# Performance work log

Measured on AMD Instinct MI355X. Metric: run time of the kernel, lower is better.

## Reference

```python
import jax, jax.numpy as jnp
import numpy as np

D_MODEL, N_HEADS, D_K, D_V, D_FF, N_LAYERS = 512, 8, 64, 64, 2048, 6
NEG = -1e9
EPS = 1e-5


def layernorm(x):
    # nn.LayerNorm(d_model) created fresh each call: weight=1, bias=0
    mu = jnp.mean(x, axis=-1, keepdims=True)
    var = jnp.var(x, axis=-1, keepdims=True)
    return (x - mu) * jax.lax.rsqrt(var + EPS)


def sinusoidal_pe(seq_len, d_model, dtype=jnp.float32):
    pos = np.arange(seq_len)[:, None].astype(np.float64)
    div = np.exp(np.arange(0, d_model, 2).astype(np.float64) * (-np.log(10000.0) / d_model))
    pe = np.zeros((seq_len, d_model))
    pe[:, 0::2] = np.sin(pos * div)
    pe[:, 1::2] = np.cos(pos * div)
    return jnp.asarray(pe, dtype=dtype)


def mha(q_in, k_in, v_in, mask, Wq, Wk, Wv, Wo):
    # q_in: [B,Lq,D]; k_in/v_in: [B,Lk,D]; mask: [B,Lq,Lk] bool (True = masked)
    B, Lq, _ = q_in.shape
    Lk = k_in.shape[1]
    Q = (q_in @ Wq).reshape(B, Lq, N_HEADS, D_K).transpose(0, 2, 1, 3)
    K = (k_in @ Wk).reshape(B, Lk, N_HEADS, D_K).transpose(0, 2, 1, 3)
    V = (v_in @ Wv).reshape(B, Lk, N_HEADS, D_V).transpose(0, 2, 1, 3)
    scores = jnp.einsum('bhqd,bhkd->bhqk', Q, K) / jnp.sqrt(jnp.asarray(D_K, q_in.dtype))
    scores = jnp.where(mask[:, None, :, :], jnp.asarray(NEG, scores.dtype), scores)
    attn = jax.nn.softmax(scores, axis=-1)
    ctx = jnp.einsum('bhqk,bhkd->bhqd', attn, V)
    ctx = ctx.transpose(0, 2, 1, 3).reshape(B, Lq, N_HEADS * D_V)
    return layernorm(ctx @ Wo + q_in)


def setup_inputs() -> dict:
    key = jax.random.key(0)
    ks = jax.random.split(key, 16)
    B, T, S, V = 8, 1024, 1024, 32000
    s = 0.02
    inp = {
        'dec_inputs': jax.random.randint(ks[0], (B, T), 0, V),
        'enc_inputs': jax.random.randint(ks[1], (B, S), 0, V),
        'enc_outputs': jax.random.normal(ks[2], (B, S, D_MODEL), jnp.float32),
        'emb': jax.random.normal(ks[3], (V, D_MODEL), jnp.float32) * s,
        'Wq_self': jax.random.normal(ks[4], (N_LAYERS, D_MODEL, N_HEADS * D_K), jnp.float32) * s,
        'Wk_self': jax.random.normal(ks[5], (N_LAYERS, D_MODEL, N_HEADS * D_K), jnp.float32) * s,
        'Wv_self': jax.random.normal(ks[6], (N_LAYERS, D_MODEL, N_HEADS * D_V), jnp.float32) * s,
        'Wo_self': jax.random.normal(ks[7], (N_LAYERS, N_HEADS * D_V, D_MODEL), jnp.float32) * s,
        'Wq_cross': jax.random.normal(ks[8], (N_LAYERS, D_MODEL, N_HEADS * D_K), jnp.float32) * s,
        'Wk_cross': jax.random.normal(ks[9], (N_LAYERS, D_MODEL, N_HEADS * D_K), jnp.float32) * s,
        'Wv_cross': jax.random.normal(ks[10], (N_LAYERS, D_MODEL, N_HEADS * D_V), jnp.float32) * s,
        'Wo_cross': jax.random.normal(ks[11], (N_LAYERS, N_HEADS * D_V, D_MODEL), jnp.float32) * s,
        'W1': jax.random.normal(ks[12], (N_LAYERS, D_MODEL, D_FF), jnp.float32) * s,
        'W2': jax.random.normal(ks[13], (N_LAYERS, D_FF, D_MODEL), jnp.float32) * s,
    }
    return inp


def reference(dec_inputs, enc_inputs, enc_outputs, emb, Wq_self, Wk_self, Wv_self, Wo_self,
              Wq_cross, Wk_cross, Wv_cross, Wo_cross, W1, W2):
    B, T = dec_inputs.shape
    S = enc_inputs.shape[1]
    # embedding with padding_idx=0 (row 0 forced to zero)
    emb_eff = emb.at[0].set(0.0)
    x = emb_eff[dec_inputs] + sinusoidal_pe(T, D_MODEL, emb.dtype)[None, :, :]
    # masks: True = masked
    pad_self = (dec_inputs == 0)[:, None, :]                       # [B,1,T]
    causal = jnp.triu(jnp.ones((T, T), bool), k=1)[None, :, :]     # [1,T,T]
    self_mask = pad_self | causal                                  # [B,T,T]
    enc_mask = jnp.broadcast_to((enc_inputs == 0)[:, None, :], (B, T, S))

    def layer(x, p):
        wqs, wks, wvs, wos, wqc, wkc, wvc, woc, w1, w2 = p
        x = mha(x, x, x, self_mask, wqs, wks, wvs, wos)
        x = mha(x, enc_outputs, enc_outputs, enc_mask, wqc, wkc, wvc, woc)
        h = jax.nn.relu(x @ w1) @ w2
        return layernorm(h + x), None

    params = (Wq_self, Wk_self, Wv_self, Wo_self, Wq_cross, Wk_cross, Wv_cross, Wo_cross, W1, W2)
    x, _ = jax.lax.scan(layer, x, params)
    return x
```

## Files before the change

kernel.cpp:

```cpp
#include <hip/hip_runtime.h>
#include <hip/hip_bf16.h>

#define DMODEL 512
#define NH     8
#define DHEAD  64
#define DFF    2048
#define NLAYER 6
#define BB     8
#define TT     1024
#define NTOK   (BB*TT)
#define ACTE   ((size_t)NTOK*DMODEL)

#define QSCALE 0.18033688011112042f

#define RESCALE_THR 8.0f

#define PST 80

typedef __bf16  bf16x8  __attribute__((ext_vector_type(8)));
typedef float   float4v __attribute__((ext_vector_type(4)));
typedef short   short4v __attribute__((ext_vector_type(4)));
typedef short   short8v __attribute__((ext_vector_type(8)));

__device__ __forceinline__ unsigned short f2bf(float f) {
    __hip_bfloat16 h = __float2bfloat16(f);
    return *reinterpret_cast<unsigned short*>(&h);
}

__device__ __forceinline__ void gl_lds16(const void* g, void* l) {
    __builtin_amdgcn_global_load_lds((const __attribute__((address_space(1))) void*)g,
                                     (__attribute__((address_space(3))) void*)l, 16, 0, 0);
}

struct Tr8Args {
    const float* src[8];
    unsigned short* dst[8];
    int dstL[8];
    int rowOff[8];
};
__global__ __launch_bounds__(256) void transpose8_kernel(Tr8Args a)
{
    __shared__ float tile[64][65];
    const int type = blockIdx.z / 6, lyr = blockIdx.z % 6;
    const float* src = a.src[type] + (size_t)lyr * 512 * 512;
    unsigned short* dst = a.dst[type] + (size_t)lyr * a.dstL[type];
    const int rowOff = a.rowOff[type];
    const int k0 = blockIdx.x * 64, n0 = blockIdx.y * 64;
    const int tid = threadIdx.x;
#pragma unroll
    for (int rep = 0; rep < 16; ++rep) {
        int idx = rep * 256 + tid;
        int r = idx >> 6, c = idx & 63;
        tile[r][c] = src[(size_t)(k0 + r) * 512 + n0 + c];
    }
    __syncthreads();
#pragma unroll
    for (int rep = 0; rep < 16; ++rep) {
        int idx = rep * 256 + tid;
        int r = idx >> 6, c = idx & 63;
        dst[(size_t)(rowOff + n0 + r) * 512 + k0 + c] = f2bf(tile[c][r]);
    }
}

__global__ __launch_bounds__(256) void transpose_conv_kernel(
    const float* __restrict__ W, unsigned short* __restrict__ Wt, int K, int N,
    size_t dstL, int rowOff)
{
    __shared__ float tile[64][65];
    const float* src = W + (size_t)blockIdx.z * K * N;
    unsigned short* dst = Wt + (size_t)blockIdx.z * dstL;
    const int k0 = blockIdx.x * 64, n0 = blockIdx.y * 64;
    const int tid = threadIdx.x;
#pragma unroll
    for (int rep = 0; rep < 16; ++rep) {
        int idx = rep * 256 + tid;
        int r = idx >> 6, c = idx & 63;
        tile[r][c] = src[(size_t)(k0 + r) * N + n0 + c];
    }
    __syncthreads();
#pragma unroll
    for (int rep = 0; rep < 16; ++rep) {
        int idx = rep * 256 + tid;
        int r = idx >> 6, c = idx & 63;
        dst[(size_t)(rowOff + n0 + r) * K + k0 + c] = f2bf(tile[c][r]);
    }
}

__global__ __launch_bounds__(256) void conv_bf16_kernel(
    const float* __restrict__ in, unsigned short* __restrict__ o)
{
    int i = (blockIdx.x * 256 + threadIdx.x) * 4;
    float4v v = *(const float4v*)(in + i);
    short4v w;
    w[0] = (short)f2bf(v[0]); w[1] = (short)f2bf(v[1]);
    w[2] = (short)f2bf(v[2]); w[3] = (short)f2bf(v[3]);
    *(short4v*)(o + i) = w;
}

__global__ __launch_bounds__(256) void embed_kernel(
    const int* __restrict__ dec, const float* __restrict__ emb,
    unsigned short* __restrict__ xb)
{
    const int row = blockIdx.x;
    const int t = row & (TT - 1);
    const int tid = threadIdx.x;
    const int tok = dec[row];
#pragma unroll
    for (int rep = 0; rep < 2; ++rep) {
        int c = tid + rep * 256;
        float e = (tok != 0) ? emb[(size_t)tok * DMODEL + c] : 0.f;
        int j = c >> 1;
        float freq = __expf(-(float)(2 * j) * (9.210340371976184f / 512.f));
        float ang = (float)t * freq;
        float pe = (c & 1) ? cosf(ang) : sinf(ang);
        xb[(size_t)row * DMODEL + c] = f2bf(e + pe);
    }
}

__global__ __launch_bounds__(256) void add_ln2(
    const float* __restrict__ t, unsigned short* __restrict__ xb,
    float* __restrict__ xout)
{
    const int lane = threadIdx.x & 63;
    const int row = blockIdx.x * 4 + (threadIdx.x >> 6);
    const size_t idx = (size_t)row * DMODEL + lane * 8;
    float4v t0 = *(const float4v*)(t + idx);
    float4v t1 = *(const float4v*)(t + idx + 4);
    float4v u0 = *(const float4v*)(t + ACTE + idx);
    float4v u1 = *(const float4v*)(t + ACTE + idx + 4);
    bf16x8 rb = *(const bf16x8*)(xb + idx);
    float v[8];
#pragma unroll
    for (int k = 0; k < 4; ++k) {
        v[k] = t0[k] + u0[k] + (float)rb[k];
        v[4 + k] = t1[k] + u1[k] + (float)rb[4 + k];
    }
    float s = 0.f, sq = 0.f;
#pragma unroll
    for (int k = 0; k < 8; ++k) { s += v[k]; sq += v[k] * v[k]; }
#pragma unroll
    for (int o = 1; o < 64; o <<= 1) { s += __shfl_xor(s, o); sq += __shfl_xor(sq, o); }
    float mu = s * (1.f / 512.f);
    float var = sq * (1.f / 512.f) - mu * mu;
    float rstd = rsqrtf(var + 1e-5f);
    if (xout) {
        float4v y0, y1;
#pragma unroll
        for (int k = 0; k < 4; ++k) { y0[k] = (v[k] - mu) * rstd; y1[k] = (v[4 + k] - mu) * rstd; }
        *(float4v*)(xout + idx) = y0;
        *(float4v*)(xout + idx + 4) = y1;
    } else {
        short8v w;
#pragma unroll
        for (int k = 0; k < 8; ++k) w[k] = (short)f2bf((v[k] - mu) * rstd);
        *(short8v*)(xb + idx) = w;
    }
}

template <int EPI, int SPLITK = 1>
__global__ __launch_bounds__(256) void gemm_bt(
    const unsigned short* __restrict__ A,
    const unsigned short* __restrict__ Bt,
    float* __restrict__ Cf,
    unsigned short* __restrict__ Cb,
    int M, int N, int K)
{
    __shared__ __attribute__((aligned(16))) short As[128 * 32];
    __shared__ __attribute__((aligned(16))) short Bs[128 * 32];
    const int tid = threadIdx.x;
    const int lane = tid & 63, wv = tid >> 6;
    const int quad = lane >> 4, l15 = lane & 15;
    const int m0 = blockIdx.x * 128, n0 = blockIdx.y * 128;
    const int wm = wv & 1, wn = wv >> 1;

    float4v acc[4][4];
#pragma unroll
    for (int i = 0; i < 4; ++i)
#pragma unroll
        for (int j = 0; j < 4; ++j) acc[i][j] = (float4v){0.f, 0.f, 0.f, 0.f};

    const int Kc = K / SPLITK;
    const int kbeg = (SPLITK > 1) ? (int)blockIdx.z * Kc : 0;
    for (int k0 = kbeg; k0 < kbeg + Kc; k0 += 32) {
#pragma unroll
        for (int i = 0; i < 2; ++i) {
            const int inst = wv * 2 + i;
            const int row = inst * 16 + (lane >> 2);
            const int cb = (lane & 3) ^ ((row >> 1) & 3);
            gl_lds16(A + (size_t)(m0 + row) * K + k0 + cb * 8, (char*)As + inst * 1024);
            gl_lds16(Bt + (size_t)(n0 + row) * K + k0 + cb * 8, (char*)Bs + inst * 1024);
        }
        __syncthreads();
        bf16x8 a[4], b[4];
#pragma unroll
        for (int i = 0; i < 4; ++i) {
            const int r = wm * 64 + i * 16 + l15;
            const int st = quad ^ ((r >> 1) & 3);
            a[i] = *(const bf16x8*)&As[r * 32 + st * 8];
        }
#pragma unroll
        for (int j = 0; j < 4; ++j) {
            const int r = wn * 64 + j * 16 + l15;
            const int st = quad ^ ((r >> 1) & 3);
            b[j] = *(const bf16x8*)&Bs[r * 32 + st * 8];
        }
#pragma unroll
        for (int i = 0; i < 4; ++i)
#pragma unroll
            for (int j = 0; j < 4; ++j)
                acc[i][j] = __builtin_amdgcn_mfma_f32_16x16x32_bf16(a[i], b[j], acc[i][j], 0, 0, 0);
        __syncthreads();
    }

    const size_t zoff = (SPLITK > 1) ? (size_t)blockIdx.z * ACTE : 0;
#pragma unroll
    for (int i = 0; i < 4; ++i) {
        const int row_base = m0 + wm * 64 + i * 16 + quad * 4;
#pragma unroll
        for (int j = 0; j < 4; ++j) {
            const int col = n0 + wn * 64 + j * 16 + l15;
#pragma unroll
            for (int r = 0; r < 4; ++r) {
                const int row = row_base + r;
                const float v = acc[i][j][r];
                if (EPI == 0) {
                    Cf[zoff + (size_t)row * N + col] = v;
                } else if (EPI == 1) {
                    Cb[(size_t)row * N + col] = f2bf(fmaxf(v, 0.f));
                } else if (EPI == 2) {
                    const int which = col >> 9;
                    const float sc = (which == 0) ? QSCALE : 1.f;
                    const int b_ = row >> 10, t = row & (TT - 1);
                    const int h = (col >> 6) & 7, d = col & 63;
                    Cb[(size_t)which * ACTE + (((size_t)(b_ * NH + h)) * TT + t) * DHEAD + d] = f2bf(v * sc);
                } else {
                    const int layer = col >> 10, which = (col >> 9) & 1;
                    const int b_ = row >> 10, t = row & (TT - 1);
                    const int h = (col >> 6) & 7, d = col & 63;
                    Cb[(size_t)(layer * 2 + which) * ACTE +
                       (((size_t)(b_ * NH + h)) * TT + t) * DHEAD + d] = f2bf(v);
                }
            }
        }
    }
}

template <bool CAUSAL>
__global__ __launch_bounds__(256, 2) void attn_kernel(
    const unsigned short* __restrict__ Q,
    const unsigned short* __restrict__ Kb,
    const unsigned short* __restrict__ Vb,
    const int* __restrict__ tokens,
    unsigned short* __restrict__ ctx)
{
    __shared__ __attribute__((aligned(16))) short Ks[2][64 * 64];
    __shared__ __attribute__((aligned(16))) short Vt[2][64 * 64];
    __shared__ __attribute__((aligned(16))) short Pl[2][4][16 * PST];
    __shared__ __attribute__((aligned(16))) float alph[2][4][16];

    const int tid = threadIdx.x, lane = tid & 63, wv = tid >> 6;
    const int quad = lane >> 4, l15 = lane & 15;
    const int p = blockIdx.y;
    const int bh = blockIdx.x;
    const int b = bh >> 3, h = bh & 7;
    const size_t kvbase = (size_t)bh * TT * DHEAD;

    const int qt0 = p;
    const int qt1 = CAUSAL ? (15 - p) : (p + 8);
    const int qg0 = qt0 * 64 + wv * 16 + l15;
    const int qg1 = qt1 * 64 + wv * 16 + l15;

    const bf16x8 qa0 = *(const bf16x8*)&Q[kvbase + (size_t)qg0 * DHEAD + quad * 8];
    const bf16x8 qa1 = *(const bf16x8*)&Q[kvbase + (size_t)qg0 * DHEAD + 32 + quad * 8];
    const bf16x8 qb0 = *(const bf16x8*)&Q[kvbase + (size_t)qg1 * DHEAD + quad * 8];
    const bf16x8 qb1 = *(const bf16x8*)&Q[kvbase + (size_t)qg1 * DHEAD + 32 + quad * 8];

    float4v O0[4], O1[4];
#pragma unroll
    for (int j = 0; j < 4; ++j) { O0[j] = (float4v){0.f,0.f,0.f,0.f}; O1[j] = (float4v){0.f,0.f,0.f,0.f}; }
    float m0_ = -INFINITY, l0_ = 0.f, m1_ = -INFINITY, l1_ = 0.f;

    const int key0 = (lane & 31) * 2;
    const int d0 = (lane >> 5) * 8 + wv * 16;
    auto stageK = [&](int kt_, int buf) {
#pragma unroll
        for (int i = 0; i < 2; ++i) {
            const int inst = wv * 2 + i;
            const int row = inst * 8 + (lane >> 3);
            const int cb = (lane & 7) ^ (row & 7);
            gl_lds16(Kb + kvbase + (size_t)(kt_ * 64 + row) * DHEAD + cb * 8,
                     (char*)Ks[buf] + inst * 1024);
        }
    };
    auto loadV = [&](int kt_, short8v& r0, short8v& r1) {
        const unsigned short* vp = Vb + kvbase + (size_t)(kt_ * 64 + key0) * DHEAD + d0;
        r0 = *(const short8v*)vp;
        r1 = *(const short8v*)(vp + DHEAD);
    };
    auto writeV = [&](int buf, const short8v& r0, const short8v& r1) {
        const int kc = key0 >> 3, ko = key0 & 7;
#pragma unroll
        for (int j = 0; j < 8; ++j) {
            const int d = d0 + j;
            unsigned pk = (unsigned)(unsigned short)r0[j] |
                          ((unsigned)(unsigned short)r1[j] << 16);
            *(unsigned*)&Vt[buf][d * 64 + ((kc ^ (d & 7)) << 3) + ko] = pk;
        }
    };

    int kt = 0;
    bf16x8 kf[4][2], vf[4][2];

    auto process = [&](int ch, const bf16x8& qf0, const bf16x8& qf1, int qg,
                       float& m, float& l, float4v* O, unsigned long long kbits) {
        float4v st[4];
        __builtin_amdgcn_s_setprio(1);
#pragma unroll
        for (int i = 0; i < 4; ++i) {
            float4v z = (float4v){0.f, 0.f, 0.f, 0.f};
            z = __builtin_amdgcn_mfma_f32_16x16x32_bf16(kf[i][0], qf0, z, 0, 0, 0);
            z = __builtin_amdgcn_mfma_f32_16x16x32_bf16(kf[i][1], qf1, z, 0, 0, 0);
            st[i] = z;
        }
        __builtin_amdgcn_s_setprio(0);
        unsigned long long mask = kbits;
        if (CAUSAL && kt * 64 + 63 > qg) {
            const int qcol = qg & 63;
            mask |= (qcol == 63) ? 0ull : (~0ull << (qcol + 1));
        }
        float sv[16], smax = -INFINITY;
#pragma unroll
        for (int i = 0; i < 4; ++i)
#pragma unroll
            for (int r = 0; r < 4; ++r) {
                const int kl = i * 16 + quad * 4 + r;
                float s = ((mask >> kl) & 1ull) ? -1e9f : st[i][r];
                sv[i * 4 + r] = s;
                smax = fmaxf(smax, s);
            }
        smax = fmaxf(smax, __shfl_xor(smax, 16));
        smax = fmaxf(smax, __shfl_xor(smax, 32));
        const bool resc = !__all(smax - m <= RESCALE_THR);
        const float mnew = resc ? fmaxf(m, smax) : m;
        float tsum = 0.f;
#pragma unroll
        for (int i = 0; i < 16; ++i) {
            float pv = __builtin_amdgcn_exp2f(sv[i] - mnew);
            sv[i] = pv; tsum += pv;
        }
        tsum += __shfl_xor(tsum, 16);
        tsum += __shfl_xor(tsum, 32);
#pragma unroll
        for (int i = 0; i < 4; ++i) {
            short4v pw;
#pragma unroll
            for (int r = 0; r < 4; ++r) pw[r] = (short)f2bf(sv[i * 4 + r]);
            *(short4v*)&Pl[ch][wv][l15 * PST + i * 16 + quad * 4] = pw;
        }
        if (resc) {
            const float alpha = __builtin_amdgcn_exp2f(m - mnew);
            l = l * alpha + tsum;
            m = mnew;
            if (lane < 16) alph[ch][wv][lane] = alpha;
            const float4v aw = *(const float4v*)&alph[ch][wv][quad * 4];
#pragma unroll
            for (int j = 0; j < 4; ++j) O[j] = O[j] * aw;
        } else {
            l += tsum;
        }
        const bf16x8 p0 = *(const bf16x8*)&Pl[ch][wv][l15 * PST + quad * 8];
        const bf16x8 p1 = *(const bf16x8*)&Pl[ch][wv][l15 * PST + 32 + quad * 8];
        __builtin_amdgcn_s_setprio(1);
#pragma unroll
        for (int j = 0; j < 4; ++j) {
            float4v o = O[j];
            o = __builtin_amdgcn_mfma_f32_16x16x32_bf16(p0, vf[j][0], o, 0, 0, 0);
            o = __builtin_amdgcn_mfma_f32_16x16x32_bf16(p1, vf[j][1], o, 0, 0, 0);
            O[j] = o;
        }
        __builtin_amdgcn_s_setprio(0);
    };

    const int nkt = CAUSAL ? (qt1 + 1) : 16;

    stageK(0, 0);
    {
        short8v v0a, v0b;
        loadV(0, v0a, v0b);
        writeV(0, v0a, v0b);
    }
    int tok_cur = tokens[(size_t)b * TT + lane];
    __syncthreads();

    short8v vn0, vn1;
    int tok_next = 0;
    for (kt = 0; kt < nkt; ++kt) {
        const int cur = kt & 1, nxt = cur ^ 1;
        const bool more = (kt + 1 < nkt);
        if (more) {
            stageK(kt + 1, nxt);
            loadV(kt + 1, vn0, vn1);
            tok_next = tokens[(size_t)b * TT + (kt + 1) * 64 + lane];
        }
        const unsigned long long kbits = __ballot(tok_cur == 0);

#pragma unroll
        for (int i = 0; i < 4; ++i) {
            const int row = i * 16 + l15;
            const int s0 = quad ^ (row & 7);
            const int s1 = (4 + quad) ^ (row & 7);
            kf[i][0] = *(const bf16x8*)&Ks[cur][row * 64 + s0 * 8];
            kf[i][1] = *(const bf16x8*)&Ks[cur][row * 64 + s1 * 8];
            vf[i][0] = *(const bf16x8*)&Vt[cur][row * 64 + s0 * 8];
            vf[i][1] = *(const bf16x8*)&Vt[cur][row * 64 + s1 * 8];
        }

        if (!CAUSAL || kt <= qt0) process(0, qa0, qa1, qg0, m0_, l0_, O0, kbits);
        process(1, qb0, qb1, qg1, m1_, l1_, O1, kbits);

        if (more) {
            writeV(nxt, vn0, vn1);
            tok_cur = tok_next;
        }
        __syncthreads();
    }

    auto finalize = [&](int ch, float l, float4v* O, int qt) {
        if (lane < 16) alph[ch][wv][lane] = l;
        const float4v lw = *(const float4v*)&alph[ch][wv][quad * 4];
        float rl[4];
#pragma unroll
        for (int r = 0; r < 4; ++r) rl[r] = __builtin_amdgcn_rcpf(lw[r]);
#pragma unroll
        for (int j = 0; j < 4; ++j)
#pragma unroll
            for (int r = 0; r < 4; ++r) {
                const int qrow = qt * 64 + wv * 16 + quad * 4 + r;
                ctx[((size_t)b * TT + qrow) * DMODEL + h * DHEAD + j * 16 + l15] =
                    f2bf(O[j][r] * rl[r]);
            }
    };
    finalize(0, l0_, O0, qt0);
    finalize(1, l1_, O1, qt1);
}

extern "C" void kernel_launch(void* const* d_in, const int* in_sizes, int n_in,
                              void* d_out, int out_size, void* d_ws, size_t ws_size,
                              hipStream_t stream)
{
    const int* dec = (const int*)d_in[0];
    const int* enc = (const int*)d_in[1];
    const float* enc_out = (const float*)d_in[2];
    const float* emb = (const float*)d_in[3];
    const float* Wq_s = (const float*)d_in[4];
    const float* Wk_s = (const float*)d_in[5];
    const float* Wv_s = (const float*)d_in[6];
    const float* Wo_s = (const float*)d_in[7];
    const float* Wq_c = (const float*)d_in[8];
    const float* Wk_c = (const float*)d_in[9];
    const float* Wv_c = (const float*)d_in[10];
    const float* Wo_c = (const float*)d_in[11];
    const float* W1 = (const float*)d_in[12];
    const float* W2 = (const float*)d_in[13];
    float* out = (float*)d_out;

    char* p = (char*)d_ws;
    auto carve = [&](size_t bytes) -> char* {
        char* r = p;
        p += (bytes + 255) & ~(size_t)255;
        return r;
    };
    unsigned short* xb   = (unsigned short*)carve(ACTE * 2);
    float* tmp1          = (float*)carve(2 * ACTE * 4);
    unsigned short* qkvb = (unsigned short*)carve(3 * ACTE * 2);
    unsigned short* ctxb = (unsigned short*)carve(ACTE * 2);
    unsigned short* encb = (unsigned short*)carve(ACTE * 2);
    unsigned short* h1   = (unsigned short*)carve((size_t)NTOK * DFF * 2);
    unsigned short* wqkvT = (unsigned short*)carve((size_t)NLAYER * 1536 * 512 * 2);
    unsigned short* woT   = (unsigned short*)carve((size_t)NLAYER * 512 * 512 * 2);
    unsigned short* wqcT  = (unsigned short*)carve((size_t)NLAYER * 512 * 512 * 2);
    unsigned short* wkvcT = (unsigned short*)carve((size_t)NLAYER * 1024 * 512 * 2);
    unsigned short* wocT  = (unsigned short*)carve((size_t)NLAYER * 512 * 512 * 2);
    unsigned short* w1T   = (unsigned short*)carve((size_t)NLAYER * 2048 * 512 * 2);
    unsigned short* w2T   = (unsigned short*)carve((size_t)NLAYER * 512 * 2048 * 2);
    const size_t used = (size_t)(p - (char*)d_ws);
    const bool pre = (used + 12 * ACTE * 2 + 256) <= ws_size;
    unsigned short* KVc = pre ? (unsigned short*)carve(12 * ACTE * 2) : nullptr;

    Tr8Args ta;
    ta.src[0] = Wq_s; ta.dst[0] = wqkvT; ta.dstL[0] = 1536 * 512; ta.rowOff[0] = 0;
    ta.src[1] = Wk_s; ta.dst[1] = wqkvT; ta.dstL[1] = 1536 * 512; ta.rowOff[1] = 512;
    ta.src[2] = Wv_s; ta.dst[2] = wqkvT; ta.dstL[2] = 1536 * 512; ta.rowOff[2] = 1024;
    ta.src[3] = Wo_s; ta.dst[3] = woT;   ta.dstL[3] = 512 * 512;  ta.rowOff[3] = 0;
    ta.src[4] = Wq_c; ta.dst[4] = wqcT;  ta.dstL[4] = 512 * 512;  ta.rowOff[4] = 0;
    ta.src[5] = Wk_c; ta.dst[5] = wkvcT; ta.dstL[5] = 1024 * 512; ta.rowOff[5] = 0;
    ta.src[6] = Wv_c; ta.dst[6] = wkvcT; ta.dstL[6] = 1024 * 512; ta.rowOff[6] = 512;
    ta.src[7] = Wo_c; ta.dst[7] = wocT;  ta.dstL[7] = 512 * 512;  ta.rowOff[7] = 0;
    transpose8_kernel<<<dim3(8, 8, 48), 256, 0, stream>>>(ta);
    transpose_conv_kernel<<<dim3(8, 32, NLAYER), 256, 0, stream>>>(W1, w1T, 512, 2048, (size_t)2048 * 512, 0);
    transpose_conv_kernel<<<dim3(32, 8, NLAYER), 256, 0, stream>>>(W2, w2T, 2048, 512, (size_t)512 * 2048, 0);
    conv_bf16_kernel<<<(int)(ACTE / 1024), 256, 0, stream>>>(enc_out, encb);
    embed_kernel<<<NTOK, 256, 0, stream>>>(dec, emb, xb);

    if (pre)
        gemm_bt<3><<<dim3(64, 48), 256, 0, stream>>>(encb, wkvcT, nullptr, KVc, NTOK, 6144, 512);

    for (int lyr = 0; lyr < NLAYER; ++lyr) {
        const unsigned short* wqkv = wqkvT + (size_t)lyr * 1536 * 512;
        const unsigned short* wo   = woT + (size_t)lyr * 512 * 512;
        const unsigned short* wqc  = wqcT + (size_t)lyr * 512 * 512;
        const unsigned short* wkvc = wkvcT + (size_t)lyr * 1024 * 512;
        const unsigned short* woc  = wocT + (size_t)lyr * 512 * 512;
        const unsigned short* w1   = w1T + (size_t)lyr * 2048 * 512;
        const unsigned short* w2   = w2T + (size_t)lyr * 512 * 2048;

        gemm_bt<2><<<dim3(64, 12), 256, 0, stream>>>(xb, wqkv, nullptr, qkvb, NTOK, 1536, 512);
        attn_kernel<true><<<dim3(BB * NH, 8), 256, 0, stream>>>(
            qkvb, qkvb + ACTE, qkvb + 2 * ACTE, dec, ctxb);
        gemm_bt<0, 2><<<dim3(64, 4, 2), 256, 0, stream>>>(ctxb, wo, tmp1, nullptr, NTOK, 512, 512);
        add_ln2<<<NTOK / 4, 256, 0, stream>>>(tmp1, xb, nullptr);

        gemm_bt<2><<<dim3(64, 4), 256, 0, stream>>>(xb, wqc, nullptr, qkvb, NTOK, 512, 512);
        const unsigned short* Kc;
        if (pre) {
            Kc = KVc + (size_t)lyr * 2 * ACTE;
        } else {
            gemm_bt<2><<<dim3(64, 8), 256, 0, stream>>>(encb, wkvc, nullptr, qkvb + ACTE, NTOK, 1024, 512);
            Kc = qkvb + ACTE;
        }
        attn_kernel<false><<<dim3(BB * NH, 8), 256, 0, stream>>>(
            qkvb, Kc, Kc + ACTE, enc, ctxb);
        gemm_bt<0, 2><<<dim3(64, 4, 2), 256, 0, stream>>>(ctxb, woc, tmp1, nullptr, NTOK, 512, 512);
        add_ln2<<<NTOK / 4, 256, 0, stream>>>(tmp1, xb, nullptr);

        gemm_bt<1><<<dim3(64, 16), 256, 0, stream>>>(xb, w1, nullptr, h1, NTOK, 2048, 512);
        gemm_bt<0, 2><<<dim3(64, 4, 2), 256, 0, stream>>>(h1, w2, tmp1, nullptr, NTOK, 512, 2048);
        add_ln2<<<NTOK / 4, 256, 0, stream>>>(tmp1, xb, (lyr == NLAYER - 1) ? out : nullptr);
    }
    (void)in_sizes; (void)n_in; (void)out_size;
}
```

Before: 1.610 ms.

## Keep attention P in registers via key permutation, one query tile per block

Loads K rows in a permuted order (sigma64) so the score MFMA output lanes line up with the A-operand layout of the PV MFMA. The probabilities then stay in registers instead of round-tripping through LDS. Each block now handles a single 64-query tile, with twice as many blocks and a higher occupancy target (4 blocks/CU), in place of pairing two tiles per block. It also skips the per-element masking when a tile has no padded keys and no causal diagonal. The cost is less K/V reuse per staged tile and a possible load imbalance in the causal case, now that tiles are no longer paired.

Result: faster. 1.560 ms (-3.1%).

```diff
diff --git a/kernel.cpp b/kernel.cpp
--- a/kernel.cpp
+++ b/kernel.cpp
@@ -15,8 +15,6 @@
 
 #define RESCALE_THR 8.0f
 
-#define PST 80
-
 typedef __bf16  bf16x8  __attribute__((ext_vector_type(8)));
 typedef float   float4v __attribute__((ext_vector_type(4)));
 typedef short   short4v __attribute__((ext_vector_type(4)));
@@ -30,6 +28,10 @@
 __device__ __forceinline__ void gl_lds16(const void* g, void* l) {
     __builtin_amdgcn_global_load_lds((const __attribute__((address_space(1))) void*)g,
                                      (__attribute__((address_space(3))) void*)l, 16, 0, 0);
+}
+
+__device__ __forceinline__ int sigma64(int x) {
+    return (x & 32) | ((x & 12) << 1) | ((x & 16) >> 2) | (x & 3);
 }
 
 struct Tr8Args {
@@ -246,7 +248,7 @@
 }
 
 template <bool CAUSAL>
-__global__ __launch_bounds__(256, 2) void attn_kernel(
+__global__ __launch_bounds__(256, 4) void attn_kernel(
     const unsigned short* __restrict__ Q,
     const unsigned short* __restrict__ Kb,
     const unsigned short* __restrict__ Vb,
@@ -255,30 +257,26 @@
 {
     __shared__ __attribute__((aligned(16))) short Ks[2][64 * 64];
     __shared__ __attribute__((aligned(16))) short Vt[2][64 * 64];
-    __shared__ __attribute__((aligned(16))) short Pl[2][4][16 * PST];
-    __shared__ __attribute__((aligned(16))) float alph[2][4][16];
 
     const int tid = threadIdx.x, lane = tid & 63, wv = tid >> 6;
     const int quad = lane >> 4, l15 = lane & 15;
-    const int p = blockIdx.y;
     const int bh = blockIdx.x;
+    const int qt = CAUSAL ? (15 - (int)blockIdx.y) : (int)blockIdx.y;
     const int b = bh >> 3, h = bh & 7;
     const size_t kvbase = (size_t)bh * TT * DHEAD;
 
-    const int qt0 = p;
-    const int qt1 = CAUSAL ? (15 - p) : (p + 8);
-    const int qg0 = qt0 * 64 + wv * 16 + l15;
-    const int qg1 = qt1 * 64 + wv * 16 + l15;
-
-    const bf16x8 qa0 = *(const bf16x8*)&Q[kvbase + (size_t)qg0 * DHEAD + quad * 8];
-    const bf16x8 qa1 = *(const bf16x8*)&Q[kvbase + (size_t)qg0 * DHEAD + 32 + quad * 8];
-    const bf16x8 qb0 = *(const bf16x8*)&Q[kvbase + (size_t)qg1 * DHEAD + quad * 8];
-    const bf16x8 qb1 = *(const bf16x8*)&Q[kvbase + (size_t)qg1 * DHEAD + 32 + quad * 8];
-
-    float4v O0[4], O1[4];
-#pragma unroll
-    for (int j = 0; j < 4; ++j) { O0[j] = (float4v){0.f,0.f,0.f,0.f}; O1[j] = (float4v){0.f,0.f,0.f,0.f}; }
-    float m0_ = -INFINITY, l0_ = 0.f, m1_ = -INFINITY, l1_ = 0.f;
+    const int qcol = wv * 16 + l15;
+    const int qg = qt * 64 + qcol;
+
+    const bf16x8 qa0 = *(const bf16x8*)&Q[kvbase + (size_t)qg * DHEAD + quad * 8];
+    const bf16x8 qa1 = *(const bf16x8*)&Q[kvbase + (size_t)qg * DHEAD + 32 + quad * 8];
+
+    float4v O[4];
+#pragma unroll
+    for (int j = 0; j < 4; ++j) O[j] = (float4v){0.f, 0.f, 0.f, 0.f};
+    float m_ = -INFINITY, l_ = 0.f;
+
+    const int sig = sigma64(lane);
 
     const int key0 = (lane & 31) * 2;
     const int d0 = (lane >> 5) * 8 + wv * 16;
@@ -288,7 +286,7 @@
             const int inst = wv * 2 + i;
             const int row = inst * 8 + (lane >> 3);
             const int cb = (lane & 7) ^ (row & 7);
-            gl_lds16(Kb + kvbase + (size_t)(kt_ * 64 + row) * DHEAD + cb * 8,
+            gl_lds16(Kb + kvbase + (size_t)(kt_ * 64 + sigma64(row)) * DHEAD + cb * 8,
                      (char*)Ks[buf] + inst * 1024);
         }
     };
@@ -308,80 +306,7 @@
         }
     };
 
-    int kt = 0;
-    bf16x8 kf[4][2], vf[4][2];
-
-    auto process = [&](int ch, const bf16x8& qf0, const bf16x8& qf1, int qg,
-                       float& m, float& l, float4v* O, unsigned long long kbits) {
-        float4v st[4];
-        __builtin_amdgcn_s_setprio(1);
-#pragma unroll
-        for (int i = 0; i < 4; ++i) {
-            float4v z = (float4v){0.f, 0.f, 0.f, 0.f};
-            z = __builtin_amdgcn_mfma_f32_16x16x32_bf16(kf[i][0], qf0, z, 0, 0, 0);
-            z = __builtin_amdgcn_mfma_f32_16x16x32_bf16(kf[i][1], qf1, z, 0, 0, 0);
-            st[i] = z;
-        }
-        __builtin_amdgcn_s_setprio(0);
-        unsigned long long mask = kbits;
-        if (CAUSAL && kt * 64 + 63 > qg) {
-            const int qcol = qg & 63;
-            mask |= (qcol == 63) ? 0ull : (~0ull << (qcol + 1));
-        }
-        float sv[16], smax = -INFINITY;
-#pragma unroll
-        for (int i = 0; i < 4; ++i)
-#pragma unroll
-            for (int r = 0; r < 4; ++r) {
-                const int kl = i * 16 + quad * 4 + r;
-                float s = ((mask >> kl) & 1ull) ? -1e9f : st[i][r];
-                sv[i * 4 + r] = s;
-                smax = fmaxf(smax, s);
-            }
-        smax = fmaxf(smax, __shfl_xor(smax, 16));
-        smax = fmaxf(smax, __shfl_xor(smax, 32));
-        const bool resc = !__all(smax - m <= RESCALE_THR);
-        const float mnew = resc ? fmaxf(m, smax) : m;
-        float tsum = 0.f;
-#pragma unroll
-        for (int i = 0; i < 16; ++i) {
-            float pv = __builtin_amdgcn_exp2f(sv[i] - mnew);
-            sv[i] = pv; tsum += pv;
-        }
-        tsum += __shfl_xor(tsum, 16);
-        tsum += __shfl_xor(tsum, 32);
-#pragma unroll
-        for (int i = 0; i < 4; ++i) {
-            short4v pw;
-#pragma unroll
-            for (int r = 0; r < 4; ++r) pw[r] = (short)f2bf(sv[i * 4 + r]);
-            *(short4v*)&Pl[ch][wv][l15 * PST + i * 16 + quad * 4] = pw;
-        }
-        if (resc) {
-            const float alpha = __builtin_amdgcn_exp2f(m - mnew);
-            l = l * alpha + tsum;
-            m = mnew;
-            if (lane < 16) alph[ch][wv][lane] = alpha;
-            const float4v aw = *(const float4v*)&alph[ch][wv][quad * 4];
-#pragma unroll
-            for (int j = 0; j < 4; ++j) O[j] = O[j] * aw;
-        } else {
-            l += tsum;
-        }
-        const bf16x8 p0 = *(const bf16x8*)&Pl[ch][wv][l15 * PST + quad * 8];
-        const bf16x8 p1 = *(const bf16x8*)&Pl[ch][wv][l15 * PST + 32 + quad * 8];
-        __builtin_amdgcn_s_setprio(1);
-#pragma unroll
-        for (int j = 0; j < 4; ++j) {
-            float4v o = O[j];
-            o = __builtin_amdgcn_mfma_f32_16x16x32_bf16(p0, vf[j][0], o, 0, 0, 0);
-            o = __builtin_amdgcn_mfma_f32_16x16x32_bf16(p1, vf[j][1], o, 0, 0, 0);
-            O[j] = o;
-        }
-        __builtin_amdgcn_s_setprio(0);
-    };
-
-    const int nkt = CAUSAL ? (qt1 + 1) : 16;
+    const int nkt = CAUSAL ? (qt + 1) : 16;
 
     stageK(0, 0);
     {
@@ -389,34 +314,109 @@
         loadV(0, v0a, v0b);
         writeV(0, v0a, v0b);
     }
-    int tok_cur = tokens[(size_t)b * TT + lane];
+    int tok_cur = tokens[(size_t)b * TT + sig];
     __syncthreads();
 
     short8v vn0, vn1;
     int tok_next = 0;
-    for (kt = 0; kt < nkt; ++kt) {
+    for (int kt = 0; kt < nkt; ++kt) {
         const int cur = kt & 1, nxt = cur ^ 1;
         const bool more = (kt + 1 < nkt);
         if (more) {
             stageK(kt + 1, nxt);
             loadV(kt + 1, vn0, vn1);
-            tok_next = tokens[(size_t)b * TT + (kt + 1) * 64 + lane];
+            tok_next = tokens[(size_t)b * TT + (kt + 1) * 64 + sig];
         }
         const unsigned long long kbits = __ballot(tok_cur == 0);
 
+        float4v st[4];
+        __builtin_amdgcn_s_setprio(1);
 #pragma unroll
         for (int i = 0; i < 4; ++i) {
             const int row = i * 16 + l15;
-            const int s0 = quad ^ (row & 7);
-            const int s1 = (4 + quad) ^ (row & 7);
-            kf[i][0] = *(const bf16x8*)&Ks[cur][row * 64 + s0 * 8];
-            kf[i][1] = *(const bf16x8*)&Ks[cur][row * 64 + s1 * 8];
-            vf[i][0] = *(const bf16x8*)&Vt[cur][row * 64 + s0 * 8];
-            vf[i][1] = *(const bf16x8*)&Vt[cur][row * 64 + s1 * 8];
-        }
-
-        if (!CAUSAL || kt <= qt0) process(0, qa0, qa1, qg0, m0_, l0_, O0, kbits);
-        process(1, qb0, qb1, qg1, m1_, l1_, O1, kbits);
+            const int x = row & 7;
+            const bf16x8 k0 = *(const bf16x8*)&Ks[cur][row * 64 + ((quad ^ x)) * 8];
+            const bf16x8 k1 = *(const bf16x8*)&Ks[cur][row * 64 + (((4 + quad) ^ x)) * 8];
+            float4v z = (float4v){0.f, 0.f, 0.f, 0.f};
+            z = __builtin_amdgcn_mfma_f32_16x16x32_bf16(k0, qa0, z, 0, 0, 0);
+            z = __builtin_amdgcn_mfma_f32_16x16x32_bf16(k1, qa1, z, 0, 0, 0);
+            st[i] = z;
+        }
+        __builtin_amdgcn_s_setprio(0);
+
+        const bool diag = CAUSAL && (kt == qt);
+        const bool domask = (kbits != 0ull) || diag;
+        float sv[16], smax = -INFINITY;
+        if (domask) {
+#pragma unroll
+            for (int i = 0; i < 4; ++i)
+#pragma unroll
+                for (int r = 0; r < 4; ++r) {
+                    const int kl = i * 16 + quad * 4 + r;
+                    const int klocal = sigma64(kl);
+                    const bool mk = ((kbits >> kl) & 1ull) || (diag && klocal > qcol);
+                    const float s = mk ? -1e9f : st[i][r];
+                    sv[i * 4 + r] = s;
+                    smax = fmaxf(smax, s);
+                }
+        } else {
+#pragma unroll
+            for (int i = 0; i < 4; ++i)
+#pragma unroll
+                for (int r = 0; r < 4; ++r) {
+                    const float s = st[i][r];
+                    sv[i * 4 + r] = s;
+                    smax = fmaxf(smax, s);
+                }
+        }
+        smax = fmaxf(smax, __shfl_xor(smax, 16));
+        smax = fmaxf(smax, __shfl_xor(smax, 32));
+        const bool resc = !__all(smax - m_ <= RESCALE_THR);
+        const float mnew = resc ? fmaxf(m_, smax) : m_;
+        float tsum = 0.f;
+#pragma unroll
+        for (int i = 0; i < 16; ++i) {
+            float pv = __builtin_amdgcn_exp2f(sv[i] - mnew);
+            sv[i] = pv; tsum += pv;
+        }
+        tsum += __shfl_xor(tsum, 16);
+        tsum += __shfl_xor(tsum, 32);
+
+        short8v pw0, pw1;
+#pragma unroll
+        for (int t = 0; t < 8; ++t) {
+            pw0[t] = (short)f2bf(sv[t]);
+            pw1[t] = (short)f2bf(sv[8 + t]);
+        }
+        const bf16x8 p0 = *reinterpret_cast<const bf16x8*>(&pw0);
+        const bf16x8 p1 = *reinterpret_cast<const bf16x8*>(&pw1);
+
+        if (resc) {
+            const float alpha = __builtin_amdgcn_exp2f(m_ - mnew);
+            l_ = l_ * alpha + tsum;
+            m_ = mnew;
+            float4v av;
+#pragma unroll
+            for (int r = 0; r < 4; ++r) av[r] = __shfl(alpha, quad * 4 + r);
+#pragma unroll
+            for (int j = 0; j < 4; ++j) O[j] = O[j] * av;
+        } else {
+            l_ += tsum;
+        }
+
+        __builtin_amdgcn_s_setprio(1);
+#pragma unroll
+        for (int j = 0; j < 4; ++j) {
+            const int row = j * 16 + l15;
+            const int x = row & 7;
+            const bf16x8 v0 = *(const bf16x8*)&Vt[cur][row * 64 + ((quad ^ x)) * 8];
+            const bf16x8 v1 = *(const bf16x8*)&Vt[cur][row * 64 + (((4 + quad) ^ x)) * 8];
+            float4v o = O[j];
+            o = __builtin_amdgcn_mfma_f32_16x16x32_bf16(p0, v0, o, 0, 0, 0);
+            o = __builtin_amdgcn_mfma_f32_16x16x32_bf16(p1, v1, o, 0, 0, 0);
+            O[j] = o;
+        }
+        __builtin_amdgcn_s_setprio(0);
 
         if (more) {
             writeV(nxt, vn0, vn1);
@@ -425,9 +425,10 @@
         __syncthreads();
     }
 
-    auto finalize = [&](int ch, float l, float4v* O, int qt) {
-        if (lane < 16) alph[ch][wv][lane] = l;
-        const float4v lw = *(const float4v*)&alph[ch][wv][quad * 4];
+    {
+        float4v lw;
+#pragma unroll
+        for (int r = 0; r < 4; ++r) lw[r] = __shfl(l_, quad * 4 + r);
         float rl[4];
 #pragma unroll
         for (int r = 0; r < 4; ++r) rl[r] = __builtin_amdgcn_rcpf(lw[r]);
@@ -439,9 +440,7 @@
                 ctx[((size_t)b * TT + qrow) * DMODEL + h * DHEAD + j * 16 + l15] =
                     f2bf(O[j][r] * rl[r]);
             }
-    };
-    finalize(0, l0_, O0, qt0);
-    finalize(1, l1_, O1, qt1);
+    }
 }
 
 extern "C" void kernel_launch(void* const* d_in, const int* in_sizes, int n_in,
@@ -515,7 +514,7 @@
         const unsigned short* w2   = w2T + (size_t)lyr * 512 * 2048;
 
         gemm_bt<2><<<dim3(64, 12), 256, 0, stream>>>(xb, wqkv, nullptr, qkvb, NTOK, 1536, 512);
-        attn_kernel<true><<<dim3(BB * NH, 8), 256, 0, stream>>>(
+        attn_kernel<true><<<dim3(BB * NH, 16), 256, 0, stream>>>(
             qkvb, qkvb + ACTE, qkvb + 2 * ACTE, dec, ctxb);
         gemm_bt<0, 2><<<dim3(64, 4, 2), 256, 0, stream>>>(ctxb, wo, tmp1, nullptr, NTOK, 512, 512);
         add_ln2<<<NTOK / 4, 256, 0, stream>>>(tmp1, xb, nullptr);
@@ -528,7 +527,7 @@
             gemm_bt<2><<<dim3(64, 8), 256, 0, stream>>>(encb, wkvc, nullptr, qkvb + ACTE, NTOK, 1024, 512);
             Kc = qkvb + ACTE;
         }
-        attn_kernel<false><<<dim3(BB * NH, 8), 256, 0, stream>>>(
+        attn_kernel<false><<<dim3(BB * NH, 16), 256, 0, stream>>>(
             qkvb, Kc, Kc + ACTE, enc, ctxb);
         gemm_bt<0, 2><<<dim3(64, 4, 2), 256, 0, stream>>>(ctxb, woc, tmp1, nullptr, NTOK, 512, 512);
         add_ln2<<<NTOK / 4, 256, 0, stream>>>(tmp1, xb, nullptr);
```
